# Optimization experiments

Hardware: AMD Instinct MI355X
Metric: run time of the kernel (lower is better)

## Reference

```python
import jax, jax.numpy as jnp
import numpy as np

N = 500_000   # nodes
D = 128       # feature dim (init arg d)
B = 1024      # number of graphs / segments
EPS = 1e-6


def setup_inputs() -> dict:
    key = jax.random.key(0)
    k_x, k_b, k_ps, k_qs, k_w, k_bias = jax.random.split(key, 6)
    x = jax.random.normal(k_x, (N, D), dtype=jnp.float32)
    batch = jnp.sort(jax.random.randint(k_b, (N,), 0, B)).astype(jnp.int64)
    ps_raw = jax.random.normal(k_ps, (2,), dtype=jnp.float32)
    qs_raw = jax.random.normal(k_qs, (2,), dtype=jnp.float32)
    W = jax.random.normal(k_w, (D, D), dtype=jnp.float32) / np.sqrt(D)
    b = jax.random.normal(k_bias, (D,), dtype=jnp.float32) * 0.01
    return {"x": x, "batch": batch, "ps_raw": ps_raw, "qs_raw": qs_raw, "W": W, "b": b}


def reference(x, batch, ps_raw, qs_raw, W, b):
    # ps = -Threshold(thr=-50, val=50)(-softplus(ps_raw))
    sp = jax.nn.softplus(ps_raw)
    ps = -jnp.where(-sp > -50.0, -sp, 50.0)
    qs = jnp.tanh(qs_raw)

    # per-graph node counts: global_add_pool(ones)
    nums = jax.ops.segment_sum(jnp.ones(x.shape[0], dtype=x.dtype), batch,
                               num_segments=B)[:, None]            # (B, 1)

    xa = jnp.abs(x) + EPS                                           # (N, D)
    d1 = xa.shape[1] // 2                                           # split feature dim

    # positive branch: exp(p0 * log(x)) == x**p0, summed per graph
    x_pos = jnp.exp(ps[0] * jnp.log(xa[:, :d1]))                    # (N, d1)
    s_pos = jax.ops.segment_sum(x_pos, batch, num_segments=B)       # (B, d1)
    gnp_pos = jnp.exp(jnp.log(s_pos) / ps[0]) / nums ** qs[0]

    # negative branch: plain power / root p-norm form
    s_neg = jax.ops.segment_sum(xa[:, d1:] ** ps[1], batch, num_segments=B)  # (B, D-d1)
    gnp_neg = s_neg ** (1.0 / ps[1]) / nums ** qs[0]

    gnp = jnp.concatenate([gnp_pos, gnp_neg], axis=1)               # (B, D)
    return gnp @ W.T + b
```

## Files before the change

kernel.cpp:

```cpp
#include <hip/hip_runtime.h>
#include <math.h>

#define NSEG   1024
#define DFEAT  128
#define EPS_F  1e-6f
#define NBLK_A 2048
#define THR_A  256

__device__ __forceinline__ float softplus_thr(float v) {
    float sp = log1pf(__expf(v));
    return (sp >= 50.0f) ? -50.0f : sp;
}

__global__ __launch_bounds__(THR_A, 8)
void segsum_chunk_kernel(const float* __restrict__ x,
                         const int*   __restrict__ batch,
                         const float* __restrict__ ps_raw,
                         float* __restrict__ pcF,
                         float* __restrict__ pcL,
                         int*   __restrict__ idFL,
                         float* __restrict__ sMid,
                         int n_nodes, int chunk)
{
    const int k   = blockIdx.x;
    const int tid = threadIdx.x;
    const int hw  = tid >> 5;
    const int f4  = tid & 31;
    const int r0  = k * chunk;

    if (r0 >= n_nodes) {
        if (tid == 0) { idFL[2 * k] = -1; idFL[2 * k + 1] = -1; }
        return;
    }
    const int r1  = min(r0 + chunk, n_nodes);
    const int idF = batch[r0];
    const int idL = batch[r1 - 1];
    if (tid == 0) { idFL[2 * k] = idF; idFL[2 * k + 1] = idL; }

    for (int sg = idF + 1 + hw; sg < idL; sg += 8) {
        float4* p = (float4*)&sMid[(size_t)sg * DFEAT];
        p[f4] = make_float4(0.f, 0.f, 0.f, 0.f);
    }
    __syncthreads();

    const float p = softplus_thr(ps_raw[(f4 < 16) ? 0 : 1]);
    const float4* __restrict__ x4 = (const float4*)x;

    float4 aF  = make_float4(0.f, 0.f, 0.f, 0.f);
    float4 aL  = make_float4(0.f, 0.f, 0.f, 0.f);
    float4 acc = make_float4(0.f, 0.f, 0.f, 0.f);

    auto flush = [&](int seg) {
        if (seg == idF) {
            aF.x += acc.x; aF.y += acc.y; aF.z += acc.z; aF.w += acc.w;
        } else if (seg == idL) {
            aL.x += acc.x; aL.y += acc.y; aL.z += acc.z; aL.w += acc.w;
        } else {
            float* base = &sMid[(size_t)seg * DFEAT + 4 * f4];
            atomicAdd(base + 0, acc.x); atomicAdd(base + 1, acc.y);
            atomicAdd(base + 2, acc.z); atomicAdd(base + 3, acc.w);
        }
        acc = make_float4(0.f, 0.f, 0.f, 0.f);
    };

    int rfirst = r0 + hw;
    int cur = (rfirst < r1) ? batch[rfirst] : idF;

#pragma unroll 2
    for (int r = rfirst; r < r1; r += 8) {
        const int sg = batch[r];
        if (sg != cur) { flush(cur); cur = sg; }
        const float4 v = x4[(size_t)r * 32 + f4];
        acc.x += __expf(p * __logf(fabsf(v.x) + EPS_F));
        acc.y += __expf(p * __logf(fabsf(v.y) + EPS_F));
        acc.z += __expf(p * __logf(fabsf(v.z) + EPS_F));
        acc.w += __expf(p * __logf(fabsf(v.w) + EPS_F));
    }
    flush(cur);

    __shared__ float pFs[8][DFEAT];
    __shared__ float pLs[8][DFEAT];
    *(float4*)&pFs[hw][4 * f4] = aF;
    *(float4*)&pLs[hw][4 * f4] = aL;
    __syncthreads();

    if (tid < DFEAT) {
        float sF = 0.f, sL = 0.f;
#pragma unroll
        for (int j = 0; j < 8; ++j) { sF += pFs[j][tid]; sL += pLs[j][tid]; }
        pcF[(size_t)k * DFEAT + tid] = sF;
        pcL[(size_t)k * DFEAT + tid] = sL;
    }
}

__global__ __launch_bounds__(128)
void finalize_gemm_kernel(const int*   __restrict__ batch,
                          const float* __restrict__ pcF,
                          const float* __restrict__ pcL,
                          const int*   __restrict__ idFL,
                          const float* __restrict__ sMid,
                          const float* __restrict__ ps_raw,
                          const float* __restrict__ qs_raw,
                          const float* __restrict__ W,
                          const float* __restrict__ bias,
                          float* __restrict__ out,
                          int n_nodes, int chunk, int nblk)
{
    const int b = blockIdx.x;
    const int i = threadIdx.x;

    int lo0 = 0, hi0 = n_nodes, lo1 = 0, hi1 = n_nodes;
    while (lo0 < hi0) { int m = (lo0 + hi0) >> 1; if (batch[m] < b)     lo0 = m + 1; else hi0 = m; }
    while (lo1 < hi1) { int m = (lo1 + hi1) >> 1; if (batch[m] < b + 1) lo1 = m + 1; else hi1 = m; }
    const int start = lo0, end = lo1;

    float ssum = 0.f;
    if (end > start) {
        const int ks = start / chunk;
        const int ke = (end - 1) / chunk;
        for (int k = ks; k <= ke && k < nblk; ++k) {
            const int f = idFL[2 * k], l = idFL[2 * k + 1];
            if (f == b)                 ssum += pcF[(size_t)k * DFEAT + i];
            else if (f < b && b < l)    ssum += sMid[(size_t)b * DFEAT + i];
            if (l == b && l != f)       ssum += pcL[(size_t)k * DFEAT + i];
        }
    }

    __shared__ float g[DFEAT];
    const float pf = softplus_thr(ps_raw[(i < 64) ? 0 : 1]);
    const float q0 = tanhf(qs_raw[0]);
    const float n  = (float)(end - start);
    g[i] = __expf(__logf(ssum) / pf - q0 * __logf(n));
    __syncthreads();

    const float4* __restrict__ W4 = (const float4*)(W + (size_t)i * DFEAT);
    const float4* g4 = (const float4*)g;
    float acc = bias[i];
#pragma unroll
    for (int jj = 0; jj < DFEAT / 4; ++jj) {
        const float4 wv = W4[jj];
        const float4 gv = g4[jj];
        acc += gv.x * wv.x + gv.y * wv.y + gv.z * wv.z + gv.w * wv.w;
    }
    out[(size_t)b * DFEAT + i] = acc;
}

extern "C" void kernel_launch(void* const* d_in, const int* in_sizes, int n_in,
                              void* d_out, int out_size, void* d_ws, size_t ws_size,
                              hipStream_t stream)
{
    const float* x      = (const float*)d_in[0];
    const int*   batch  = (const int*)  d_in[1];
    const float* ps_raw = (const float*)d_in[2];
    const float* qs_raw = (const float*)d_in[3];
    const float* W      = (const float*)d_in[4];
    const float* bias   = (const float*)d_in[5];
    float*       out    = (float*)d_out;

    const int n_nodes = in_sizes[0] / DFEAT;
    const int chunk   = (n_nodes + NBLK_A - 1) / NBLK_A;

    float* pcF  = (float*)d_ws;
    float* pcL  = pcF  + (size_t)NBLK_A * DFEAT;
    float* sMid = pcL  + (size_t)NBLK_A * DFEAT;
    int*   idFL = (int*)(sMid + (size_t)NSEG * DFEAT);

    segsum_chunk_kernel<<<NBLK_A, THR_A, 0, stream>>>(
        x, batch, ps_raw, pcF, pcL, idFL, sMid, n_nodes, chunk);
    finalize_gemm_kernel<<<NSEG, 128, 0, stream>>>(
        batch, pcF, pcL, idFL, sMid, ps_raw, qs_raw, W, bias, out,
        n_nodes, chunk, NBLK_A);
}
```

Baseline: 374.9 us.

## Precompute segment boundaries in chunk kernel and drop per-row batch reads

Measured after the change: 368.4 us. About the same (-1.7%).

```diff
diff --git a/kernel.cpp b/kernel.cpp
--- a/kernel.cpp
+++ b/kernel.cpp
@@ -20,6 +20,7 @@
                          float* __restrict__ pcL,
                          int*   __restrict__ idFL,
                          float* __restrict__ sMid,
+                         int*   __restrict__ segStart,
                          int n_nodes, int chunk)
 {
     const int k   = blockIdx.x;
@@ -27,56 +28,62 @@
     const int hw  = tid >> 5;
     const int f4  = tid & 31;
     const int r0  = k * chunk;
+    if (r0 >= n_nodes) return;
 
-    if (r0 >= n_nodes) {
-        if (tid == 0) { idFL[2 * k] = -1; idFL[2 * k + 1] = -1; }
-        return;
-    }
-    const int r1  = min(r0 + chunk, n_nodes);
-    const int idF = batch[r0];
-    const int idL = batch[r1 - 1];
+    const int r1   = min(r0 + chunk, n_nodes);
+    const int idF  = batch[r0];
+    const int idL  = batch[r1 - 1];
+    const int prev = (k == 0) ? -1 : batch[r0 - 1];
     if (tid == 0) { idFL[2 * k] = idF; idFL[2 * k + 1] = idL; }
 
+    for (int s = prev + 1 + tid; s <= idF; s += THR_A) segStart[s] = r0;
+    if (r1 == n_nodes)
+        for (int s = idL + 1 + tid; s <= NSEG; s += THR_A) segStart[s] = n_nodes;
+
     for (int sg = idF + 1 + hw; sg < idL; sg += 8) {
-        float4* p = (float4*)&sMid[(size_t)sg * DFEAT];
-        p[f4] = make_float4(0.f, 0.f, 0.f, 0.f);
+        float4* pz = (float4*)&sMid[(size_t)sg * DFEAT];
+        pz[f4] = make_float4(0.f, 0.f, 0.f, 0.f);
     }
-    __syncthreads();
+    if (idL > idF + 1) __syncthreads();
 
     const float p = softplus_thr(ps_raw[(f4 < 16) ? 0 : 1]);
     const float4* __restrict__ x4 = (const float4*)x;
 
-    float4 aF  = make_float4(0.f, 0.f, 0.f, 0.f);
-    float4 aL  = make_float4(0.f, 0.f, 0.f, 0.f);
-    float4 acc = make_float4(0.f, 0.f, 0.f, 0.f);
+    float4 aF = make_float4(0.f, 0.f, 0.f, 0.f);
+    float4 aL = make_float4(0.f, 0.f, 0.f, 0.f);
 
-    auto flush = [&](int seg) {
-        if (seg == idF) {
+    int a = r0;
+    for (int s = idF; s <= idL; ++s) {
+        int bnd;
+        if (s == idL) bnd = r1;
+        else {
+            int lo = a + 1, hi = r1;
+            while (lo < hi) { int m = (lo + hi) >> 1; if (batch[m] < s + 1) lo = m + 1; else hi = m; }
+            bnd = lo;
+            if (tid == 0) segStart[s + 1] = bnd;
+        }
+
+        float4 acc = make_float4(0.f, 0.f, 0.f, 0.f);
+#pragma unroll 2
+        for (int r = a + hw; r < bnd; r += 8) {
+            const float4 v = x4[(size_t)r * 32 + f4];
+            acc.x += __expf(p * __logf(fabsf(v.x) + EPS_F));
+            acc.y += __expf(p * __logf(fabsf(v.y) + EPS_F));
+            acc.z += __expf(p * __logf(fabsf(v.z) + EPS_F));
+            acc.w += __expf(p * __logf(fabsf(v.w) + EPS_F));
+        }
+
+        if (s == idF) {
             aF.x += acc.x; aF.y += acc.y; aF.z += acc.z; aF.w += acc.w;
-        } else if (seg == idL) {
+        } else if (s == idL) {
             aL.x += acc.x; aL.y += acc.y; aL.z += acc.z; aL.w += acc.w;
         } else {
-            float* base = &sMid[(size_t)seg * DFEAT + 4 * f4];
+            float* base = &sMid[(size_t)s * DFEAT + 4 * f4];
             atomicAdd(base + 0, acc.x); atomicAdd(base + 1, acc.y);
             atomicAdd(base + 2, acc.z); atomicAdd(base + 3, acc.w);
         }
-        acc = make_float4(0.f, 0.f, 0.f, 0.f);
-    };
-
-    int rfirst = r0 + hw;
-    int cur = (rfirst < r1) ? batch[rfirst] : idF;
-
-#pragma unroll 2
-    for (int r = rfirst; r < r1; r += 8) {
-        const int sg = batch[r];
-        if (sg != cur) { flush(cur); cur = sg; }
-        const float4 v = x4[(size_t)r * 32 + f4];
-        acc.x += __expf(p * __logf(fabsf(v.x) + EPS_F));
-        acc.y += __expf(p * __logf(fabsf(v.y) + EPS_F));
-        acc.z += __expf(p * __logf(fabsf(v.z) + EPS_F));
-        acc.w += __expf(p * __logf(fabsf(v.w) + EPS_F));
+        a = bnd;
     }
-    flush(cur);
 
     __shared__ float pFs[8][DFEAT];
     __shared__ float pLs[8][DFEAT];
@@ -94,25 +101,23 @@
 }
 
 __global__ __launch_bounds__(128)
-void finalize_gemm_kernel(const int*   __restrict__ batch,
-                          const float* __restrict__ pcF,
+void finalize_gemm_kernel(const float* __restrict__ pcF,
                           const float* __restrict__ pcL,
                           const int*   __restrict__ idFL,
                           const float* __restrict__ sMid,
+                          const int*   __restrict__ segStart,
                           const float* __restrict__ ps_raw,
                           const float* __restrict__ qs_raw,
                           const float* __restrict__ W,
                           const float* __restrict__ bias,
                           float* __restrict__ out,
-                          int n_nodes, int chunk, int nblk)
+                          int chunk, int nblk)
 {
     const int b = blockIdx.x;
     const int i = threadIdx.x;
 
-    int lo0 = 0, hi0 = n_nodes, lo1 = 0, hi1 = n_nodes;
-    while (lo0 < hi0) { int m = (lo0 + hi0) >> 1; if (batch[m] < b)     lo0 = m + 1; else hi0 = m; }
-    while (lo1 < hi1) { int m = (lo1 + hi1) >> 1; if (batch[m] < b + 1) lo1 = m + 1; else hi1 = m; }
-    const int start = lo0, end = lo1;
+    const int start = segStart[b];
+    const int end   = segStart[b + 1];
 
     float ssum = 0.f;
     if (end > start) {
@@ -120,9 +125,9 @@
         const int ke = (end - 1) / chunk;
         for (int k = ks; k <= ke && k < nblk; ++k) {
             const int f = idFL[2 * k], l = idFL[2 * k + 1];
-            if (f == b)                 ssum += pcF[(size_t)k * DFEAT + i];
-            else if (f < b && b < l)    ssum += sMid[(size_t)b * DFEAT + i];
-            if (l == b && l != f)       ssum += pcL[(size_t)k * DFEAT + i];
+            if (f == b)              ssum += pcF[(size_t)k * DFEAT + i];
+            else if (f < b && b < l) ssum += sMid[(size_t)b * DFEAT + i];
+            if (l == b && l != f)    ssum += pcL[(size_t)k * DFEAT + i];
         }
     }
 
@@ -160,14 +165,15 @@
     const int n_nodes = in_sizes[0] / DFEAT;
     const int chunk   = (n_nodes + NBLK_A - 1) / NBLK_A;
 
-    float* pcF  = (float*)d_ws;
-    float* pcL  = pcF  + (size_t)NBLK_A * DFEAT;
-    float* sMid = pcL  + (size_t)NBLK_A * DFEAT;
-    int*   idFL = (int*)(sMid + (size_t)NSEG * DFEAT);
+    float* pcF      = (float*)d_ws;
+    float* pcL      = pcF  + (size_t)NBLK_A * DFEAT;
+    float* sMid     = pcL  + (size_t)NBLK_A * DFEAT;
+    int*   idFL     = (int*)(sMid + (size_t)NSEG * DFEAT);
+    int*   segStart = idFL + (size_t)NBLK_A * 2;
 
     segsum_chunk_kernel<<<NBLK_A, THR_A, 0, stream>>>(
-        x, batch, ps_raw, pcF, pcL, idFL, sMid, n_nodes, chunk);
+        x, batch, ps_raw, pcF, pcL, idFL, sMid, segStart, n_nodes, chunk);
     finalize_gemm_kernel<<<NSEG, 128, 0, stream>>>(
-        batch, pcF, pcL, idFL, sMid, ps_raw, qs_raw, W, bias, out,
-        n_nodes, chunk, NBLK_A);
+        pcF, pcL, idFL, sMid, segStart, ps_raw, qs_raw, W, bias, out,
+        chunk, NBLK_A);
 }
```
